# Kernel tuning notes

Hardware: AMD Instinct MI355X
Metric: run time of the kernel (lower is better)

The kernel has to match this reference:

```python
import jax, jax.numpy as jnp
import numpy as np

BLOCK_SIZES = [256] * 8            # sum = N_CTX = 2048
B, H, D = 2, 16, 64
N_CTX = sum(BLOCK_SIZES)
SPARSITY_PATTERN = 'block_causal'  # row_starts = 0, row_ends = end of own block


def _build_masks(block_sizes, pattern):
    cs = np.cumsum([0] + list(block_sizes))
    row_ends = np.concatenate([np.full(bs, cs[i + 1], dtype=np.int32)
                               for i, bs in enumerate(block_sizes)])
    if pattern == 'block_diagonal':
        row_starts = np.concatenate([np.full(bs, cs[i], dtype=np.int32)
                                     for i, bs in enumerate(block_sizes)])
    elif pattern == 'block_causal':
        row_starts = np.zeros_like(row_ends)
    else:
        raise ValueError(pattern)
    return jnp.asarray(row_starts), jnp.asarray(row_ends)


def setup_inputs() -> dict:
    key = jax.random.key(0)
    kq, kk, kv = jax.random.split(key, 3)
    q = jax.random.normal(kq, (B, H, N_CTX, D), dtype=jnp.float32)
    k = jax.random.normal(kk, (B, H, N_CTX, D), dtype=jnp.float32)
    v = jax.random.normal(kv, (B, H, N_CTX, D), dtype=jnp.float32)
    row_starts, row_ends = _build_masks(BLOCK_SIZES, SPARSITY_PATTERN)
    sm_scale = jnp.float32(1.0 / np.sqrt(D))
    return {"q": q, "k": k, "v": v, "sm_scale": sm_scale,
            "row_starts": row_starts, "row_ends": row_ends}


def reference(q, k, v, sm_scale, row_starts, row_ends):
    # q,k,v: [B,H,N,D]; per query row i, attend to kv cols in [row_starts[i], row_ends[i])
    n = q.shape[2]
    cols = jnp.arange(n, dtype=jnp.int32)
    allowed = (cols[None, :] >= row_starts[:, None]) & (cols[None, :] < row_ends[:, None])  # [N,N]
    scores = jnp.einsum('bhqd,bhkd->bhqk', q, k) * sm_scale
    neg = jnp.finfo(scores.dtype).min
    scores = jnp.where(allowed[None, None], scores, neg)
    p = jax.nn.softmax(scores, axis=-1)
    return jnp.einsum('bhqk,bhkd->bhqd', p, v)
```

## Files before the change

kernel.cpp:

```cpp
#include <hip/hip_runtime.h>


typedef short bf16x8 __attribute__((ext_vector_type(8)));
typedef float f32x4  __attribute__((ext_vector_type(4)));
typedef unsigned short u16;
typedef u16 u16x8 __attribute__((ext_vector_type(8)));

#define MFMA(A,B,C) __builtin_amdgcn_mfma_f32_16x16x32_bf16((A),(B),(C),0,0,0)

__device__ __forceinline__ u16 f2bf_rne(float f) {
    union { float f; unsigned u; } c; c.f = f;
    unsigned r = c.u + 0x7FFFu + ((c.u >> 16) & 1u);
    return (u16)(r >> 16);
}
__device__ __forceinline__ u16 f2bf_fast(float f) {
    union { float f; unsigned u; } c; c.f = f;
    return (u16)((c.u + 0x8000u) >> 16);
}

__device__ __forceinline__ void gload_lds16(const void* g, void* lds) {
    __builtin_amdgcn_global_load_lds(
        (const __attribute__((address_space(1))) unsigned int*)g,
        (__attribute__((address_space(3))) unsigned int*)lds, 16, 0, 0);
}

__global__ __launch_bounds__(256)
void prep_kernel(const float* __restrict__ K, const float* __restrict__ V,
                 u16* __restrict__ blob)
{
    int bt = blockIdx.x;
    int tid = threadIdx.x;
    const size_t gbase = (size_t)bt * 4096;
    u16* bb = blob + (size_t)bt * 8192;
    __shared__ __align__(16) u16 lt[4096];
    {
        int key = tid >> 2, c2 = (tid & 3) << 1;
        int rotb = (key & 3) + 4 * ((key >> 3) & 1);
        const float* kp = K + gbase + key * 64 + c2 * 8;
        float4 x0 = *(const float4*)kp,       x1 = *(const float4*)(kp + 4);
        float4 x2 = *(const float4*)(kp + 8), x3 = *(const float4*)(kp + 12);
        u16x8 a, b;
        a[0]=f2bf_rne(x0.x); a[1]=f2bf_rne(x0.y); a[2]=f2bf_rne(x0.z); a[3]=f2bf_rne(x0.w);
        a[4]=f2bf_rne(x1.x); a[5]=f2bf_rne(x1.y); a[6]=f2bf_rne(x1.z); a[7]=f2bf_rne(x1.w);
        b[0]=f2bf_rne(x2.x); b[1]=f2bf_rne(x2.y); b[2]=f2bf_rne(x2.z); b[3]=f2bf_rne(x2.w);
        b[4]=f2bf_rne(x3.x); b[5]=f2bf_rne(x3.y); b[6]=f2bf_rne(x3.z); b[7]=f2bf_rne(x3.w);
        *(u16x8*)&bb[key * 64 + (((c2    ) + rotb) & 7) * 8] = a;
        *(u16x8*)&bb[key * 64 + (((c2 + 1) + rotb) & 7) * 8] = b;
    }
    {
        int wv = tid >> 6, ln = tid & 63;
        const float* vp = V + gbase + ln * 64 + wv * 16;
        float4 y0 = *(const float4*)vp,       y1 = *(const float4*)(vp + 4);
        float4 y2 = *(const float4*)(vp + 8), y3 = *(const float4*)(vp + 12);
        float yy[16] = { y0.x,y0.y,y0.z,y0.w, y1.x,y1.y,y1.z,y1.w,
                         y2.x,y2.y,y2.z,y2.w, y3.x,y3.y,y3.z,y3.w };
        int kc = ln >> 3, kw = ln & 7;
        #pragma unroll
        for (int j = 0; j < 16; ++j) {
            int d = wv * 16 + j;
            lt[d * 64 + ((kc + (j & 7)) & 7) * 8 + kw] = f2bf_rne(yy[j]);
        }
    }
    __syncthreads();
    {
        int o = tid * 16;
        *(u16x8*)&bb[4096 + o]     = *(const u16x8*)&lt[o];
        *(u16x8*)&bb[4096 + o + 8] = *(const u16x8*)&lt[o + 8];
    }
}

__global__ __launch_bounds__(256, 2)
void bsattn_main(const float* __restrict__ Q, const float* __restrict__ SC,
                 const int* __restrict__ RS, const int* __restrict__ RE,
                 const u16* __restrict__ blob, float* __restrict__ O)
{
    constexpr int N = 2048, D = 64;
    int wg = blockIdx.x;
    int bh = wg & 31;
    int i0 = wg >> 5;
    int qsub = (i0 < 8) ? i0 : 23 - i0;
    int q0 = qsub << 7;

    int tid = threadIdx.x, wid = tid >> 6, lane = tid & 63;
    int n = lane & 15, g = lane >> 4;

    __shared__ __align__(16) u16 lsm[16384];
    __shared__ int sbi[8];

    int row0 = q0 + wid * 32 + n;
    int row1 = row0 + 16;
    int rs_l0 = RS[row0], re_l0 = RE[row0];
    int rs_l1 = RS[row1], re_l1 = RE[row1];
    int w_rs_min = min(rs_l0, rs_l1), w_rs_max = max(rs_l0, rs_l1);
    int w_re_min = min(re_l0, re_l1), w_re_max = max(re_l0, re_l1);
    #pragma unroll
    for (int o = 1; o < 16; o <<= 1) {
        w_rs_min = min(w_rs_min, __shfl_xor(w_rs_min, o));
        w_rs_max = max(w_rs_max, __shfl_xor(w_rs_max, o));
        w_re_min = min(w_re_min, __shfl_xor(w_re_min, o));
        w_re_max = max(w_re_max, __shfl_xor(w_re_max, o));
    }
    if (lane == 0) { sbi[wid * 2] = w_rs_min; sbi[wid * 2 + 1] = w_re_max; }

    float sscale = SC[0] * 1.44269504088896340736f;

    bf16x8 qA0, qA1, qB0, qB1;
    {
        const float* qp = Q + ((size_t)bh * N + row0) * D + g * 8;
        float4 a0 = *(const float4*)qp,        a1 = *(const float4*)(qp + 4);
        float4 b0 = *(const float4*)(qp + 32), b1 = *(const float4*)(qp + 36);
        qA0[0]=f2bf_rne(a0.x*sscale); qA0[1]=f2bf_rne(a0.y*sscale);
        qA0[2]=f2bf_rne(a0.z*sscale); qA0[3]=f2bf_rne(a0.w*sscale);
        qA0[4]=f2bf_rne(a1.x*sscale); qA0[5]=f2bf_rne(a1.y*sscale);
        qA0[6]=f2bf_rne(a1.z*sscale); qA0[7]=f2bf_rne(a1.w*sscale);
        qA1[0]=f2bf_rne(b0.x*sscale); qA1[1]=f2bf_rne(b0.y*sscale);
        qA1[2]=f2bf_rne(b0.z*sscale); qA1[3]=f2bf_rne(b0.w*sscale);
        qA1[4]=f2bf_rne(b1.x*sscale); qA1[5]=f2bf_rne(b1.y*sscale);
        qA1[6]=f2bf_rne(b1.z*sscale); qA1[7]=f2bf_rne(b1.w*sscale);
    }
    {
        const float* qp = Q + ((size_t)bh * N + row1) * D + g * 8;
        float4 a0 = *(const float4*)qp,        a1 = *(const float4*)(qp + 4);
        float4 b0 = *(const float4*)(qp + 32), b1 = *(const float4*)(qp + 36);
        qB0[0]=f2bf_rne(a0.x*sscale); qB0[1]=f2bf_rne(a0.y*sscale);
        qB0[2]=f2bf_rne(a0.z*sscale); qB0[3]=f2bf_rne(a0.w*sscale);
        qB0[4]=f2bf_rne(a1.x*sscale); qB0[5]=f2bf_rne(a1.y*sscale);
        qB0[6]=f2bf_rne(a1.z*sscale); qB0[7]=f2bf_rne(a1.w*sscale);
        qB1[0]=f2bf_rne(b0.x*sscale); qB1[1]=f2bf_rne(b0.y*sscale);
        qB1[2]=f2bf_rne(b0.z*sscale); qB1[3]=f2bf_rne(b0.w*sscale);
        qB1[4]=f2bf_rne(b1.x*sscale); qB1[5]=f2bf_rne(b1.y*sscale);
        qB1[6]=f2bf_rne(b1.z*sscale); qB1[7]=f2bf_rne(b1.w*sscale);
    }

    __syncthreads();
    int kst  = min(min(sbi[0], sbi[2]), min(sbi[4], sbi[6])) & ~63;
    int kend = max(max(sbi[1], sbi[3]), max(sbi[5], sbi[7]));
    int t0 = kst >> 6;
    int w  = (kend - kst + 63) >> 6;

    int rA   = ((n >> 2) << 3) + (n & 3);
    int phk  = (n & 3) + 4 * ((n >> 2) & 1);
    int osA0 = rA * 64 + ((g + phk) & 7) * 8;
    int osA1 = rA * 64 + ((g + 4 + phk) & 7) * 8;
    int ov0  = 4096 + n * 64 + ((    g + (n & 7)) & 7) * 8;
    int ov1  = 4096 + n * 64 + ((4 + g + (n & 7)) & 7) * 8;

    f32x4 accA[4], accB[4];
    f32x4 acclA = {0.f,0.f,0.f,0.f}, acclB = {0.f,0.f,0.f,0.f};
    #pragma unroll
    for (int c = 0; c < 4; ++c) {
        accA[c] = (f32x4){0.f,0.f,0.f,0.f};
        accB[c] = (f32x4){0.f,0.f,0.f,0.f};
    }
    bf16x8 ones;
    #pragma unroll
    for (int j = 0; j < 8; ++j) ones[j] = (short)0x3F80;

    auto stage = [&](int i) {
        if (i < w) {
            const u16* src = blob + (size_t)(bh * 32 + t0 + i) * 8192;
            u16* dst = &lsm[(i & 1) << 13];
            int wb = wid * 2048;
            #pragma unroll
            for (int c = 0; c < 4; ++c)
                gload_lds16(src + wb + c * 512 + lane * 8, dst + wb + c * 512);
        }
    };

    auto proc = [&](int kb, const u16* ls) {
        bool bdry = (kb < w_rs_max) || (kb + 64 > w_re_min);
        #pragma unroll
        for (int h = 0; h < 2; ++h) {
            int hb = h * 2048;
            bf16x8 k00 = *(const bf16x8*)&ls[hb + osA0];
            bf16x8 k01 = *(const bf16x8*)&ls[hb + osA1];
            bf16x8 k10 = *(const bf16x8*)&ls[hb + osA0 + 256];
            bf16x8 k11 = *(const bf16x8*)&ls[hb + osA1 + 256];
            f32x4 tA0 = {0.f,0.f,0.f,0.f}, tA1 = tA0, tB0 = tA0, tB1 = tA0;
            __builtin_amdgcn_s_setprio(1);
            tA0 = MFMA(k00, qA0, tA0); tA0 = MFMA(k01, qA1, tA0);
            tA1 = MFMA(k10, qA0, tA1); tA1 = MFMA(k11, qA1, tA1);
            tB0 = MFMA(k00, qB0, tB0); tB0 = MFMA(k01, qB1, tB0);
            tB1 = MFMA(k10, qB0, tB1); tB1 = MFMA(k11, qB1, tB1);
            __builtin_amdgcn_s_setprio(0);
            float sA[8], sB[8];
            #pragma unroll
            for (int r = 0; r < 4; ++r) {
                sA[r] = tA0[r]; sA[4 + r] = tA1[r];
                sB[r] = tB0[r]; sB[4 + r] = tB1[r];
            }
            if (bdry) {
                #pragma unroll
                for (int j = 0; j < 8; ++j) {
                    int key = kb + h * 32 + g * 8 + j;
                    if (key < rs_l0 || key >= re_l0) sA[j] = -1e30f;
                    if (key < rs_l1 || key >= re_l1) sB[j] = -1e30f;
                }
            }
            bf16x8 pA, pB;
            #pragma unroll
            for (int j = 0; j < 8; ++j) { float p = __builtin_amdgcn_exp2f(sA[j]); pA[j] = (short)f2bf_fast(p); }
            #pragma unroll
            for (int j = 0; j < 8; ++j) { float p = __builtin_amdgcn_exp2f(sB[j]); pB[j] = (short)f2bf_fast(p); }
            int ov = h ? ov1 : ov0;
            bf16x8 v0 = *(const bf16x8*)&ls[ov       ];
            bf16x8 v1 = *(const bf16x8*)&ls[ov + 1024];
            bf16x8 v2 = *(const bf16x8*)&ls[ov + 2048];
            bf16x8 v3 = *(const bf16x8*)&ls[ov + 3072];
            __builtin_amdgcn_s_setprio(1);
            accA[0] = MFMA(pA, v0, accA[0]);
            accA[1] = MFMA(pA, v1, accA[1]);
            accA[2] = MFMA(pA, v2, accA[2]);
            accA[3] = MFMA(pA, v3, accA[3]);
            acclA   = MFMA(pA, ones, acclA);
            accB[0] = MFMA(pB, v0, accB[0]);
            accB[1] = MFMA(pB, v1, accB[1]);
            accB[2] = MFMA(pB, v2, accB[2]);
            accB[3] = MFMA(pB, v3, accB[3]);
            acclB   = MFMA(pB, ones, acclB);
            __builtin_amdgcn_s_setprio(0);
        }
    };

    stage(0);
    for (int i = 0; i < w; ++i) {
        __syncthreads();
        stage(i + 1);
        proc(kst + (i << 6), &lsm[(i & 1) << 13]);
    }

    int rb = g << 2;
    {
        int orow = q0 + wid * 32 + rb;
        float* ob = O + ((size_t)bh * N + orow) * D + n;
        #pragma unroll
        for (int r = 0; r < 4; ++r) {
            float li = 1.0f / acclA[r];
            float* rp = ob + (size_t)r * D;
            rp[0]  = accA[0][r] * li;
            rp[16] = accA[1][r] * li;
            rp[32] = accA[2][r] * li;
            rp[48] = accA[3][r] * li;
        }
    }
    {
        int orow = q0 + wid * 32 + 16 + rb;
        float* ob = O + ((size_t)bh * N + orow) * D + n;
        #pragma unroll
        for (int r = 0; r < 4; ++r) {
            float li = 1.0f / acclB[r];
            float* rp = ob + (size_t)r * D;
            rp[0]  = accB[0][r] * li;
            rp[16] = accB[1][r] * li;
            rp[32] = accB[2][r] * li;
            rp[48] = accB[3][r] * li;
        }
    }
}

extern "C" void kernel_launch(void* const* d_in, const int* in_sizes, int n_in,
                              void* d_out, int out_size, void* d_ws, size_t ws_size,
                              hipStream_t stream) {
    const float* q  = (const float*)d_in[0];
    const float* k  = (const float*)d_in[1];
    const float* v  = (const float*)d_in[2];
    const float* sc = (const float*)d_in[3];
    const int* rs   = (const int*)d_in[4];
    const int* re   = (const int*)d_in[5];
    float* out      = (float*)d_out;
    u16* blob       = (u16*)d_ws;

    prep_kernel<<<dim3(1024), dim3(256), 0, stream>>>(k, v, blob);
    bsattn_main<<<dim3(512), dim3(256), 0, stream>>>(q, sc, rs, re, blob, out);
}
```

Baseline: 135.5 us.

## Fuse K/V bf16 conversion into attention kernel with register-prefetched staging

Removes the separate prep kernel that converted K and V to swizzled bf16 in a workspace. The main kernel now loads fp32 K/V tiles into registers one iteration ahead, converts them, and writes the swizzled and transposed layout into LDS after computing the current tile. This saves one kernel launch and the workspace round trip. In exchange, each workgroup redoes the conversion for every tile it visits, global reads double in size (fp32), and register pressure and scalar LDS writes rise.

```diff
diff --git a/kernel.cpp b/kernel.cpp
--- a/kernel.cpp
+++ b/kernel.cpp
@@ -18,61 +18,11 @@
     return (u16)((c.u + 0x8000u) >> 16);
 }
 
-__device__ __forceinline__ void gload_lds16(const void* g, void* lds) {
-    __builtin_amdgcn_global_load_lds(
-        (const __attribute__((address_space(1))) unsigned int*)g,
-        (__attribute__((address_space(3))) unsigned int*)lds, 16, 0, 0);
-}
-
-__global__ __launch_bounds__(256)
-void prep_kernel(const float* __restrict__ K, const float* __restrict__ V,
-                 u16* __restrict__ blob)
-{
-    int bt = blockIdx.x;
-    int tid = threadIdx.x;
-    const size_t gbase = (size_t)bt * 4096;
-    u16* bb = blob + (size_t)bt * 8192;
-    __shared__ __align__(16) u16 lt[4096];
-    {
-        int key = tid >> 2, c2 = (tid & 3) << 1;
-        int rotb = (key & 3) + 4 * ((key >> 3) & 1);
-        const float* kp = K + gbase + key * 64 + c2 * 8;
-        float4 x0 = *(const float4*)kp,       x1 = *(const float4*)(kp + 4);
-        float4 x2 = *(const float4*)(kp + 8), x3 = *(const float4*)(kp + 12);
-        u16x8 a, b;
-        a[0]=f2bf_rne(x0.x); a[1]=f2bf_rne(x0.y); a[2]=f2bf_rne(x0.z); a[3]=f2bf_rne(x0.w);
-        a[4]=f2bf_rne(x1.x); a[5]=f2bf_rne(x1.y); a[6]=f2bf_rne(x1.z); a[7]=f2bf_rne(x1.w);
-        b[0]=f2bf_rne(x2.x); b[1]=f2bf_rne(x2.y); b[2]=f2bf_rne(x2.z); b[3]=f2bf_rne(x2.w);
-        b[4]=f2bf_rne(x3.x); b[5]=f2bf_rne(x3.y); b[6]=f2bf_rne(x3.z); b[7]=f2bf_rne(x3.w);
-        *(u16x8*)&bb[key * 64 + (((c2    ) + rotb) & 7) * 8] = a;
-        *(u16x8*)&bb[key * 64 + (((c2 + 1) + rotb) & 7) * 8] = b;
-    }
-    {
-        int wv = tid >> 6, ln = tid & 63;
-        const float* vp = V + gbase + ln * 64 + wv * 16;
-        float4 y0 = *(const float4*)vp,       y1 = *(const float4*)(vp + 4);
-        float4 y2 = *(const float4*)(vp + 8), y3 = *(const float4*)(vp + 12);
-        float yy[16] = { y0.x,y0.y,y0.z,y0.w, y1.x,y1.y,y1.z,y1.w,
-                         y2.x,y2.y,y2.z,y2.w, y3.x,y3.y,y3.z,y3.w };
-        int kc = ln >> 3, kw = ln & 7;
-        #pragma unroll
-        for (int j = 0; j < 16; ++j) {
-            int d = wv * 16 + j;
-            lt[d * 64 + ((kc + (j & 7)) & 7) * 8 + kw] = f2bf_rne(yy[j]);
-        }
-    }
-    __syncthreads();
-    {
-        int o = tid * 16;
-        *(u16x8*)&bb[4096 + o]     = *(const u16x8*)&lt[o];
-        *(u16x8*)&bb[4096 + o + 8] = *(const u16x8*)&lt[o + 8];
-    }
-}
-
 __global__ __launch_bounds__(256, 2)
-void bsattn_main(const float* __restrict__ Q, const float* __restrict__ SC,
-                 const int* __restrict__ RS, const int* __restrict__ RE,
-                 const u16* __restrict__ blob, float* __restrict__ O)
+void bsattn_fused(const float* __restrict__ Q, const float* __restrict__ K,
+                  const float* __restrict__ V, const float* __restrict__ SC,
+                  const int* __restrict__ RS, const int* __restrict__ RE,
+                  float* __restrict__ O)
 {
     constexpr int N = 2048, D = 64;
     int wg = blockIdx.x;
@@ -145,6 +95,14 @@
     int ov0  = 4096 + n * 64 + ((    g + (n & 7)) & 7) * 8;
     int ov1  = 4096 + n * 64 + ((4 + g + (n & 7)) & 7) * 8;
 
+    int key_l = tid >> 2, c2 = (tid & 3) << 1;
+    int rotb  = (key_l & 3) + 4 * ((key_l >> 3) & 1);
+    int kiA   = key_l * 64 + (((c2    ) + rotb) & 7) * 8;
+    int kiB   = key_l * 64 + (((c2 + 1) + rotb) & 7) * 8;
+    int kc    = lane >> 3, kw = lane & 7;
+    const float* Kb = K + (size_t)bh * N * D;
+    const float* Vb = V + (size_t)bh * N * D;
+
     f32x4 accA[4], accB[4];
     f32x4 acclA = {0.f,0.f,0.f,0.f}, acclB = {0.f,0.f,0.f,0.f};
     #pragma unroll
@@ -156,14 +114,35 @@
     #pragma unroll
     for (int j = 0; j < 8; ++j) ones[j] = (short)0x3F80;
 
-    auto stage = [&](int i) {
+    float4 kf0, kf1, kf2, kf3, vf0, vf1, vf2, vf3;
+
+    auto stage_load = [&](int i) {
         if (i < w) {
-            const u16* src = blob + (size_t)(bh * 32 + t0 + i) * 8192;
+            const float* kp = Kb + (size_t)(t0 + i) * 4096 + key_l * 64 + c2 * 8;
+            kf0 = *(const float4*)kp;       kf1 = *(const float4*)(kp + 4);
+            kf2 = *(const float4*)(kp + 8); kf3 = *(const float4*)(kp + 12);
+            const float* vp = Vb + (size_t)(t0 + i) * 4096 + lane * 64 + wid * 16;
+            vf0 = *(const float4*)vp;       vf1 = *(const float4*)(vp + 4);
+            vf2 = *(const float4*)(vp + 8); vf3 = *(const float4*)(vp + 12);
+        }
+    };
+    auto stage_write = [&](int i) {
+        if (i < w) {
             u16* dst = &lsm[(i & 1) << 13];
-            int wb = wid * 2048;
-            #pragma unroll
-            for (int c = 0; c < 4; ++c)
-                gload_lds16(src + wb + c * 512 + lane * 8, dst + wb + c * 512);
+            u16x8 a, b;
+            a[0]=f2bf_rne(kf0.x); a[1]=f2bf_rne(kf0.y); a[2]=f2bf_rne(kf0.z); a[3]=f2bf_rne(kf0.w);
+            a[4]=f2bf_rne(kf1.x); a[5]=f2bf_rne(kf1.y); a[6]=f2bf_rne(kf1.z); a[7]=f2bf_rne(kf1.w);
+            b[0]=f2bf_rne(kf2.x); b[1]=f2bf_rne(kf2.y); b[2]=f2bf_rne(kf2.z); b[3]=f2bf_rne(kf2.w);
+            b[4]=f2bf_rne(kf3.x); b[5]=f2bf_rne(kf3.y); b[6]=f2bf_rne(kf3.z); b[7]=f2bf_rne(kf3.w);
+            *(u16x8*)&dst[kiA] = a;
+            *(u16x8*)&dst[kiB] = b;
+            float vy[16] = { vf0.x,vf0.y,vf0.z,vf0.w, vf1.x,vf1.y,vf1.z,vf1.w,
+                             vf2.x,vf2.y,vf2.z,vf2.w, vf3.x,vf3.y,vf3.z,vf3.w };
+            #pragma unroll
+            for (int j = 0; j < 16; ++j) {
+                int d = wid * 16 + j;
+                dst[4096 + d * 64 + ((kc + (j & 7)) & 7) * 8 + kw] = f2bf_rne(vy[j]);
+            }
         }
     };
 
@@ -222,11 +201,14 @@
         }
     };
 
-    stage(0);
+    stage_load(0);
+    stage_write(0);
+    stage_load(1);
     for (int i = 0; i < w; ++i) {
         __syncthreads();
-        stage(i + 1);
         proc(kst + (i << 6), &lsm[(i & 1) << 13]);
+        stage_write(i + 1);
+        stage_load(i + 2);
     }
 
     int rb = g << 2;
@@ -268,8 +250,6 @@
     const int* rs   = (const int*)d_in[4];
     const int* re   = (const int*)d_in[5];
     float* out      = (float*)d_out;
-    u16* blob       = (u16*)d_ws;
-
-    prep_kernel<<<dim3(1024), dim3(256), 0, stream>>>(k, v, blob);
-    bsattn_main<<<dim3(512), dim3(256), 0, stream>>>(q, sc, rs, re, blob, out);
-}
+
+    bsattn_fused<<<dim3(512), dim3(256), 0, stream>>>(q, k, v, sc, rs, re, out);
+}
```

After: 130.8 us. -3.5%, faster.
